# Kernel optimization log

Hardware: AMD Instinct MI355X
Metric: run time of the kernel (lower is better)

## Reference

```python
import jax, jax.numpy as jnp
import numpy as np

N_NODES = 100000
N_EDGES = 1600000
IN_DIM = 128
HID = 128
OUT = 64


def gcn_conv(x, src, dst, W, b, n_nodes):
    # x: [N, Din] -> [N, Dout]; symmetric-normalized GCN with self-loops (PyG GCNConv defaults)
    h = x @ W  # transform first (as PyG does)
    loop = jnp.arange(n_nodes, dtype=src.dtype)
    s = jnp.concatenate([src, loop])
    d = jnp.concatenate([dst, loop])
    deg = jax.ops.segment_sum(jnp.ones_like(d, dtype=h.dtype), d, num_segments=n_nodes)
    dis = jnp.where(deg > 0, jax.lax.rsqrt(deg), 0.0)
    norm = dis[s] * dis[d]  # [E+N]
    msgs = h[s] * norm[:, None]  # gather-transform
    out = jax.ops.segment_sum(msgs, d, num_segments=n_nodes)  # scatter-add
    return out + b


def setup_inputs() -> dict:
    key = jax.random.key(0)
    ks = jax.random.split(key, 12)
    x = jax.random.normal(ks[0], (N_NODES, IN_DIM), dtype=jnp.float32)
    edge_index = jax.random.randint(ks[1], (2, N_EDGES), 0, N_NODES, dtype=jnp.int32)
    def lin(k, fan_in, fan_out):
        bound = 1.0 / np.sqrt(fan_in)
        kw, kb = jax.random.split(k)
        W = jax.random.uniform(kw, (fan_in, fan_out), minval=-bound, maxval=bound, dtype=jnp.float32)
        b = jax.random.uniform(kb, (fan_out,), minval=-bound, maxval=bound, dtype=jnp.float32)
        return W, b
    W1, b1 = lin(ks[2], IN_DIM, HID)
    W2, b2 = lin(ks[3], HID, HID)
    Wp1, bp1 = lin(ks[4], HID, HID)
    Wp2, bp2 = lin(ks[5], HID, OUT)
    return {"x": x, "edge_index": edge_index,
            "W1": W1, "b1": b1, "W2": W2, "b2": b2,
            "Wp1": Wp1, "bp1": bp1, "Wp2": Wp2, "bp2": bp2}


def reference(x, edge_index, W1, b1, W2, b2, Wp1, bp1, Wp2, bp2):
    n = x.shape[0]
    src, dst = edge_index[0], edge_index[1]
    # layer 1: GCNConv + relu (dropout inactive at eval)
    h = jax.nn.relu(gcn_conv(x, src, dst, W1, b1, n))
    # layer 2
    h = jax.nn.relu(gcn_conv(h, src, dst, W2, b2, n))
    # post MLP head
    h = h @ Wp1 + bp1
    h = h @ Wp2 + bp2
    return jax.nn.log_softmax(h, axis=1)
```

## Files before the change

kernel.cpp:

```cpp
#include <hip/hip_runtime.h>
#include <hip/hip_bf16.h>
#include <cstdint>

typedef __attribute__((ext_vector_type(8))) short short8;
typedef __attribute__((ext_vector_type(16))) float f32x16;
typedef unsigned short us;

#define BIN_SHIFT 8
#define BIN_NODES 256
#define CAPB 6144
#define EPB 4096

__device__ __forceinline__ float bflo(uint32_t u) { return __builtin_bit_cast(float, u << 16); }
__device__ __forceinline__ float bfhi(uint32_t u) { return __builtin_bit_cast(float, u & 0xffff0000u); }

__device__ __forceinline__ us f32_to_bf16_rne(float f) {
  uint32_t u = __builtin_bit_cast(uint32_t, f);
  u += 0x7fffu + ((u >> 16) & 1u);
  return (us)(u >> 16);
}

__device__ __forceinline__ void split2(float f, us& h, us& l) {
  uint32_t u = __builtin_bit_cast(uint32_t, f);
  h = (us)(u >> 16);
  float fh = __builtin_bit_cast(float, u & 0xffff0000u);
  float r = f - fh;
  l = (us)(__builtin_bit_cast(uint32_t, r) >> 16);
}

__global__ void k_prep(const float* __restrict__ W1, const float* __restrict__ W2,
                       const float* __restrict__ Wp1, const float* __restrict__ Wp2,
                       const float* __restrict__ bp1, const float* __restrict__ bp2,
                       us* __restrict__ Wt1h, us* __restrict__ Wt1l,
                       us* __restrict__ Wt2h, us* __restrict__ Wt2l,
                       us* __restrict__ Wch, us* __restrict__ Wcl, float* __restrict__ bc,
                       int* __restrict__ gcur, int* __restrict__ hzero) {
  int blk = blockIdx.x, tid = threadIdx.x;
  if (blk < 128) {
    const float* W = (blk < 64) ? W1 : W2;
    us* Wh = (blk < 64) ? Wt1h : Wt2h;
    us* Wl = (blk < 64) ? Wt1l : Wt2l;
    int idx = (blk & 63) * 256 + tid;
    int k = idx >> 7, n = idx & 127;
    us h, l;
    split2(W[idx], h, l);
    Wh[n * 128 + k] = h;
    Wl[n * 128 + k] = l;
  } else if (blk < 160) {
    int idx = (blk - 128) * 256 + tid;
    int k = idx >> 6, j = idx & 63;
    float acc = 0.f;
    for (int t = 0; t < 128; ++t) acc += Wp1[k * 128 + t] * Wp2[t * 64 + j];
    us h, l;
    split2(acc, h, l);
    Wch[j * 128 + k] = h;
    Wcl[j * 128 + k] = l;
  } else {
    gcur[tid] = 0;
    gcur[tid + 256] = 0;
    if (tid < 64) {
      hzero[tid] = 0;
      float acc = bp2[tid];
      for (int t = 0; t < 128; ++t) acc += bp1[t] * Wp2[t * 64 + tid];
      bc[tid] = acc;
    }
  }
}

__global__ __launch_bounds__(256) void k_binA(
    const int* __restrict__ src, const int* __restrict__ dst,
    uint2* __restrict__ binbuf, int* __restrict__ gcur, int E, int nbins) {
  __shared__ uint2 stage[EPB];
  __shared__ int cnt[512], base[512], cur[512], gbase[512];
  int tid = threadIdx.x;
  int e0 = blockIdx.x * EPB;
  int ne = min(EPB, E - e0);
  if (ne <= 0) return;
  cnt[tid] = 0; cnt[tid + 256] = 0;
  __syncthreads();
  for (int i = tid; i < ne; i += 256) atomicAdd(&cnt[dst[e0 + i] >> BIN_SHIFT], 1);
  __syncthreads();
  if (tid < 64) {
    int carry = 0;
#pragma unroll
    for (int c = 0; c < 8; ++c) {
      int v = cnt[c * 64 + tid];
      int incl = v;
#pragma unroll
      for (int off = 1; off < 64; off <<= 1) {
        int t = __shfl_up(incl, off, 64);
        if (tid >= off) incl += t;
      }
      base[c * 64 + tid] = carry + incl - v;
      carry += __shfl(incl, 63, 64);
    }
  }
  __syncthreads();
  for (int b = tid; b < nbins; b += 256)
    if (cnt[b] > 0) gbase[b] = atomicAdd(&gcur[b], cnt[b]);
  cur[tid] = base[tid]; cur[tid + 256] = base[tid + 256];
  __syncthreads();
  for (int i = tid; i < ne; i += 256) {
    int d = dst[e0 + i], s = src[e0 + i];
    int p = atomicAdd(&cur[d >> BIN_SHIFT], 1);
    stage[p] = make_uint2((unsigned)d, (unsigned)s);
  }
  __syncthreads();
  for (int i = tid; i < ne; i += 256) {
    uint2 en = stage[i];
    int b = en.x >> BIN_SHIFT;
    int gi = gbase[b] + (i - base[b]);
    if (gi < CAPB) binbuf[(size_t)b * CAPB + gi] = en;
  }
}

__global__ __launch_bounds__(256) void k_passB(
    const uint2* __restrict__ binbuf, const int* __restrict__ gcur,
    int* __restrict__ deg, float* __restrict__ dis, int* __restrict__ start,
    int* __restrict__ col, int N, int nbins) {
  __shared__ int hist[256], lstart[256], cur[256];
  __shared__ int colstage[CAPB];
  __shared__ int binbase_s;
  int b = blockIdx.x, tid = threadIdx.x;
  int node0 = b << BIN_SHIFT;
  int cnt = min(gcur[b], CAPB);
  hist[tid] = 0;
  __syncthreads();
  const uint2* bp = binbuf + (size_t)b * CAPB;
  for (int i = tid; i < cnt; i += 256) atomicAdd(&hist[bp[i].x & (BIN_NODES - 1)], 1);
  __syncthreads();
  if (tid < 64) {
    int s = 0;
    for (int i = tid; i < b; i += 64) s += min(gcur[i], CAPB);
#pragma unroll
    for (int off = 32; off; off >>= 1) s += __shfl_xor(s, off, 64);
    if (tid == 0) binbase_s = s;
    int carry = 0;
#pragma unroll
    for (int c = 0; c < 4; ++c) {
      int v = hist[c * 64 + tid];
      int incl = v;
#pragma unroll
      for (int off = 1; off < 64; off <<= 1) {
        int t = __shfl_up(incl, off, 64);
        if (tid >= off) incl += t;
      }
      lstart[c * 64 + tid] = carry + incl - v;
      carry += __shfl(incl, 63, 64);
    }
  }
  __syncthreads();
  int binbase = binbase_s;
  {
    int node = node0 + tid;
    if (node < N) {
      int dg = hist[tid];
      deg[node] = dg;
      dis[node] = rsqrtf((float)(dg + 1));
      start[node] = binbase + lstart[tid];
    }
  }
  cur[tid] = lstart[tid];
  __syncthreads();
  for (int i = tid; i < cnt; i += 256) {
    uint2 en = bp[i];
    int p = atomicAdd(&cur[en.x & (BIN_NODES - 1)], 1);
    colstage[p] = (int)en.y;
  }
  __syncthreads();
  for (int i = tid; i < cnt; i += 256) col[binbase + i] = colstage[i];
}

__global__ __launch_bounds__(256) void k_gemm1(
    const float* __restrict__ A, const us* __restrict__ Wh,
    const us* __restrict__ Wl, const float* __restrict__ dis,
    us* __restrict__ out_bf16, int N, int ntiles) {
  __shared__ us As[32 * 136];
  int tid = threadIdx.x;
  int wave = tid >> 6, lane = tid & 63;
  int n0 = wave * 32;
  int nn = n0 + (lane & 31);
  int khalf = (lane >> 5) * 8;
  int m = lane & 31;

  short8 bh[8], bl[8];
#pragma unroll
  for (int c = 0; c < 8; ++c) {
    bh[c] = *(const short8*)&Wh[nn * 128 + c * 16 + khalf];
    bl[c] = *(const short8*)&Wl[nn * 128 + c * 16 + khalf];
  }

  for (int t = blockIdx.x; t < ntiles; t += gridDim.x) {
    int row0 = t * 32;
    __syncthreads();
    for (int j = tid; j < 1024; j += 256) {
      int r = j >> 5, c = j & 31;
      int row = row0 + r;
      float4 v = make_float4(0.f, 0.f, 0.f, 0.f);
      if (row < N) v = *(const float4*)&A[(size_t)row * 128 + c * 4];
      *(ushort4*)&As[r * 136 + c * 4] = make_ushort4(
          f32_to_bf16_rne(v.x), f32_to_bf16_rne(v.y),
          f32_to_bf16_rne(v.z), f32_to_bf16_rne(v.w));
    }
    __syncthreads();

    f32x16 acc = {};
#pragma unroll
    for (int c = 0; c < 8; ++c) {
      short8 ah = *(const short8*)&As[m * 136 + c * 16 + khalf];
      acc = __builtin_amdgcn_mfma_f32_32x32x16_bf16(ah, bh[c], acc, 0, 0, 0);
      acc = __builtin_amdgcn_mfma_f32_32x32x16_bf16(ah, bl[c], acc, 0, 0, 0);
    }

    int col = n0 + (lane & 31);
    int rbase = row0 + 4 * (lane >> 5);
#pragma unroll
    for (int reg = 0; reg < 16; ++reg) {
      int row = rbase + (reg & 3) + 8 * (reg >> 2);
      if (row < N) {
        float v = acc[reg] * dis[row];
        out_bf16[(size_t)row * 128 + col] = f32_to_bf16_rne(v);
      }
    }
  }
}

__global__ __launch_bounds__(256) void k_gemm2(
    const us* __restrict__ A, const us* __restrict__ Wh,
    const us* __restrict__ Wl, const float* __restrict__ dis,
    us* __restrict__ out_bf16, int N, int ntiles) {
  __shared__ us As[32 * 136];
  int tid = threadIdx.x;
  int wave = tid >> 6, lane = tid & 63;
  int n0 = wave * 32;
  int nn = n0 + (lane & 31);
  int khalf = (lane >> 5) * 8;
  int m = lane & 31;

  short8 bh[8], bl[8];
#pragma unroll
  for (int c = 0; c < 8; ++c) {
    bh[c] = *(const short8*)&Wh[nn * 128 + c * 16 + khalf];
    bl[c] = *(const short8*)&Wl[nn * 128 + c * 16 + khalf];
  }

  for (int t = blockIdx.x; t < ntiles; t += gridDim.x) {
    int row0 = t * 32;
    __syncthreads();
    for (int j = tid; j < 512; j += 256) {
      int r = j >> 4, c = j & 15;
      int row = row0 + r;
      uint4 v = make_uint4(0u, 0u, 0u, 0u);
      if (row < N) v = *(const uint4*)&A[(size_t)row * 128 + c * 8];
      *(uint4*)&As[r * 136 + c * 8] = v;
    }
    __syncthreads();

    f32x16 acc = {};
#pragma unroll
    for (int c = 0; c < 8; ++c) {
      short8 ah = *(const short8*)&As[m * 136 + c * 16 + khalf];
      acc = __builtin_amdgcn_mfma_f32_32x32x16_bf16(ah, bh[c], acc, 0, 0, 0);
      acc = __builtin_amdgcn_mfma_f32_32x32x16_bf16(ah, bl[c], acc, 0, 0, 0);
    }

    int col = n0 + (lane & 31);
    int rbase = row0 + 4 * (lane >> 5);
#pragma unroll
    for (int reg = 0; reg < 16; ++reg) {
      int row = rbase + (reg & 3) + 8 * (reg >> 2);
      if (row < N) {
        float v = acc[reg] * dis[row];
        out_bf16[(size_t)row * 128 + col] = f32_to_bf16_rne(v);
      }
    }
  }
}

__global__ __launch_bounds__(512) void k_gather(
    const us* __restrict__ h, us* __restrict__ o,
    const int* __restrict__ start, const int* __restrict__ deg,
    const int* __restrict__ col, const float* __restrict__ dis,
    const float* __restrict__ bias, int N) {
  int wave = threadIdx.x >> 6, lane = threadIdx.x & 63;
  int node = blockIdx.x * 8 + wave;
  if (node >= N) return;
  const uint32_t* h1 = (const uint32_t*)h;
  uint32_t u = h1[(size_t)node * 64 + lane];
  float a0 = bflo(u), b0 = bfhi(u);
  float a1 = 0.f, b1 = 0.f, a2 = 0.f, b2 = 0.f, a3 = 0.f, b3 = 0.f;
  float a4 = 0.f, b4 = 0.f, a5 = 0.f, b5 = 0.f, a6 = 0.f, b6 = 0.f, a7 = 0.f, b7 = 0.f;
  int e0 = start[node];
  int dg = deg[node];
  int myc = (lane < dg) ? col[e0 + lane] : N;
  int dgm = min(dg, 64);
  for (int k = 0; k < dgm; k += 8) {
    int c0 = __builtin_amdgcn_readlane(myc, k);
    int c1 = __builtin_amdgcn_readlane(myc, k + 1);
    int c2 = __builtin_amdgcn_readlane(myc, k + 2);
    int c3 = __builtin_amdgcn_readlane(myc, k + 3);
    int c4 = __builtin_amdgcn_readlane(myc, k + 4);
    int c5 = __builtin_amdgcn_readlane(myc, k + 5);
    int c6 = __builtin_amdgcn_readlane(myc, k + 6);
    int c7 = __builtin_amdgcn_readlane(myc, k + 7);
    uint32_t u0 = h1[(size_t)c0 * 64 + lane];
    uint32_t u1 = h1[(size_t)c1 * 64 + lane];
    uint32_t u2 = h1[(size_t)c2 * 64 + lane];
    uint32_t u3 = h1[(size_t)c3 * 64 + lane];
    uint32_t u4 = h1[(size_t)c4 * 64 + lane];
    uint32_t u5 = h1[(size_t)c5 * 64 + lane];
    uint32_t u6 = h1[(size_t)c6 * 64 + lane];
    uint32_t u7 = h1[(size_t)c7 * 64 + lane];
    a0 += bflo(u0); b0 += bfhi(u0);
    a1 += bflo(u1); b1 += bfhi(u1);
    a2 += bflo(u2); b2 += bfhi(u2);
    a3 += bflo(u3); b3 += bfhi(u3);
    a4 += bflo(u4); b4 += bfhi(u4);
    a5 += bflo(u5); b5 += bfhi(u5);
    a6 += bflo(u6); b6 += bfhi(u6);
    a7 += bflo(u7); b7 += bfhi(u7);
  }
  for (int e = e0 + 64; e < e0 + dg; ++e) {
    uint32_t u0 = h1[(size_t)col[e] * 64 + lane];
    a0 += bflo(u0); b0 += bfhi(u0);
  }
  float sc = dis[node];
  float2 bb = ((const float2*)bias)[lane];
  float ax = ((a0 + a1) + (a2 + a3)) + ((a4 + a5) + (a6 + a7));
  float ay = ((b0 + b1) + (b2 + b3)) + ((b4 + b5) + (b6 + b7));
  float rx = fmaxf(ax * sc + bb.x, 0.f);
  float ry = fmaxf(ay * sc + bb.y, 0.f);
  ((uint32_t*)o)[(size_t)node * 64 + lane] =
      ((uint32_t)f32_to_bf16_rne(ry) << 16) | f32_to_bf16_rne(rx);
}

__global__ __launch_bounds__(256) void k_head_mfma(
    const us* __restrict__ act, const us* __restrict__ Wch,
    const us* __restrict__ Wcl, const float* __restrict__ bc,
    float* __restrict__ out, int N) {
  __shared__ us As[64 * 136];
  __shared__ float red[2][2][64];
  int tid = threadIdx.x;
  int wave = tid >> 6, lane = tid & 63;
  int rt = wave >> 1, ct = wave & 1;
  int colj = ct * 32 + (lane & 31);
  int khalf = (lane >> 5) * 8;
  int m = lane & 31;

  short8 bh[8], bl[8];
#pragma unroll
  for (int c = 0; c < 8; ++c) {
    bh[c] = *(const short8*)&Wch[colj * 128 + c * 16 + khalf];
    bl[c] = *(const short8*)&Wcl[colj * 128 + c * 16 + khalf];
  }

  int row0 = blockIdx.x * 64;
  for (int j = tid; j < 1024; j += 256) {
    int r = j >> 4, c = j & 15;
    int row = row0 + r;
    uint4 v = make_uint4(0u, 0u, 0u, 0u);
    if (row < N) v = *(const uint4*)&act[(size_t)row * 128 + c * 8];
    *(uint4*)&As[r * 136 + c * 8] = v;
  }
  __syncthreads();

  f32x16 acc = {};
  int mrow = rt * 32 + m;
#pragma unroll
  for (int c = 0; c < 8; ++c) {
    short8 ah = *(const short8*)&As[mrow * 136 + c * 16 + khalf];
    acc = __builtin_amdgcn_mfma_f32_32x32x16_bf16(ah, bh[c], acc, 0, 0, 0);
    acc = __builtin_amdgcn_mfma_f32_32x32x16_bf16(ah, bl[c], acc, 0, 0, 0);
  }

  float bcv = bc[colj];
  float lg[16], mx[16];
#pragma unroll
  for (int reg = 0; reg < 16; ++reg) {
    lg[reg] = acc[reg] + bcv;
    float v = lg[reg];
#pragma unroll
    for (int off = 16; off > 0; off >>= 1) v = fmaxf(v, __shfl_xor(v, off, 32));
    mx[reg] = v;
  }
  if ((lane & 31) == 0) {
#pragma unroll
    for (int reg = 0; reg < 16; ++reg) {
      int rl = rt * 32 + (reg & 3) + 8 * (reg >> 2) + 4 * (lane >> 5);
      red[0][ct][rl] = mx[reg];
    }
  }
  __syncthreads();

  float ex[16], sm[16];
#pragma unroll
  for (int reg = 0; reg < 16; ++reg) {
    int rl = rt * 32 + (reg & 3) + 8 * (reg >> 2) + 4 * (lane >> 5);
    float rmax = fmaxf(red[0][0][rl], red[0][1][rl]);
    ex[reg] = lg[reg] - rmax;
    float v = expf(ex[reg]);
#pragma unroll
    for (int off = 16; off > 0; off >>= 1) v += __shfl_xor(v, off, 32);
    sm[reg] = v;
  }
  if ((lane & 31) == 0) {
#pragma unroll
    for (int reg = 0; reg < 16; ++reg) {
      int rl = rt * 32 + (reg & 3) + 8 * (reg >> 2) + 4 * (lane >> 5);
      red[1][ct][rl] = sm[reg];
    }
  }
  __syncthreads();

#pragma unroll
  for (int reg = 0; reg < 16; ++reg) {
    int rl = rt * 32 + (reg & 3) + 8 * (reg >> 2) + 4 * (lane >> 5);
    int row = row0 + rl;
    if (row < N) {
      float total = red[1][0][rl] + red[1][1][rl];
      out[(size_t)row * 64 + colj] = ex[reg] - logf(total);
    }
  }
}

extern "C" void kernel_launch(void* const* d_in, const int* in_sizes, int n_in,
                              void* d_out, int out_size, void* d_ws, size_t ws_size,
                              hipStream_t stream) {
  const float* x   = (const float*)d_in[0];
  const int*   ei  = (const int*)d_in[1];
  const float* W1  = (const float*)d_in[2];
  const float* b1  = (const float*)d_in[3];
  const float* W2  = (const float*)d_in[4];
  const float* b2  = (const float*)d_in[5];
  const float* Wp1 = (const float*)d_in[6];
  const float* bp1 = (const float*)d_in[7];
  const float* Wp2 = (const float*)d_in[8];
  const float* bp2 = (const float*)d_in[9];
  float* out = (float*)d_out;

  int N = in_sizes[0] / 128;
  int E = in_sizes[1] / 2;
  const int* src = ei;
  const int* dst = ei + E;
  int nbins = (N + BIN_NODES - 1) >> BIN_SHIFT;

  float* dis   = (float*)d_ws;
  int*   deg   = (int*)(dis + N);
  int*   start = deg + N;
  int*   col   = start + N;
  int*   gcur  = col + ((E + 3) & ~3);
  us* Wt1h = (us*)(gcur + 512);
  us* Wt1l = Wt1h + 16384;
  us* Wt2h = Wt1l + 16384;
  us* Wt2l = Wt2h + 16384;
  us* Wch  = Wt2l + 16384;
  us* Wcl  = Wch + 8192;
  float* bc = (float*)(Wcl + 8192);
  uint2* binbuf = (uint2*)(bc + 80);
  us* hbuf = (us*)(binbuf + (size_t)nbins * CAPB);
  us* act  = hbuf + (size_t)(N + 1) * 128;

  k_prep<<<161, 256, 0, stream>>>(W1, W2, Wp1, Wp2, bp1, bp2,
                                  Wt1h, Wt1l, Wt2h, Wt2l, Wch, Wcl, bc,
                                  gcur, (int*)(hbuf + (size_t)N * 128));

  int ablocks = (E + EPB - 1) / EPB;
  k_binA<<<ablocks, 256, 0, stream>>>(src, dst, binbuf, gcur, E, nbins);
  k_passB<<<nbins, 256, 0, stream>>>(binbuf, gcur, deg, dis, start, col, N, nbins);

  int ntiles = (N + 31) / 32;
  int gemm_grid = ntiles < 1024 ? ntiles : 1024;
  int agblocks = (N + 7) / 8;
  int hblocks = (N + 63) / 64;

  k_gemm1<<<gemm_grid, 256, 0, stream>>>(x, Wt1h, Wt1l, dis, hbuf, N, ntiles);
  k_gather<<<agblocks, 512, 0, stream>>>(hbuf, act, start, deg, col, dis, b1, N);
  k_gemm2<<<gemm_grid, 256, 0, stream>>>(act, Wt2h, Wt2l, dis, hbuf, N, ntiles);
  k_gather<<<agblocks, 512, 0, stream>>>(hbuf, act, start, deg, col, dis, b2, N);
  k_head_mfma<<<hblocks, 256, 0, stream>>>(act, Wch, Wcl, bc, out, N);
}
```

Before: 389.2 us.

## Compute degrees via global atomics early and overlap CSR build with GEMM1

Degree counting moves out of the per-bin pass into extra k_prep blocks that do global atomicAdd on deg, and extra k_binA blocks then compute dis from it. Because dis no longer depends on the CSR pass, that pass and the first GEMM are merged into one launch (k_pg), with separate block ranges, so they run concurrently. This removes a kernel launch and a serialization point, at the cost of 1.6M global atomics and an added memset.

```diff
diff --git a/kernel.cpp b/kernel.cpp
--- a/kernel.cpp
+++ b/kernel.cpp
@@ -34,7 +34,8 @@
                        us* __restrict__ Wt1h, us* __restrict__ Wt1l,
                        us* __restrict__ Wt2h, us* __restrict__ Wt2l,
                        us* __restrict__ Wch, us* __restrict__ Wcl, float* __restrict__ bc,
-                       int* __restrict__ gcur, int* __restrict__ hzero) {
+                       int* __restrict__ gcur, int* __restrict__ hzero,
+                       const int* __restrict__ dst, int* __restrict__ deg, int E) {
   int blk = blockIdx.x, tid = threadIdx.x;
   if (blk < 128) {
     const float* W = (blk < 64) ? W1 : W2;
@@ -55,7 +56,7 @@
     split2(acc, h, l);
     Wch[j * 128 + k] = h;
     Wcl[j * 128 + k] = l;
-  } else {
+  } else if (blk == 160) {
     gcur[tid] = 0;
     gcur[tid + 256] = 0;
     if (tid < 64) {
@@ -64,12 +65,23 @@
       for (int t = 0; t < 128; ++t) acc += bp1[t] * Wp2[t * 64 + tid];
       bc[tid] = acc;
     }
+  } else {
+    int e0 = (blk - 161) * EPB;
+    int ne = min(EPB, E - e0);
+    for (int i = tid; i < ne; i += 256) atomicAdd(&deg[dst[e0 + i]], 1);
   }
 }
 
 __global__ __launch_bounds__(256) void k_binA(
     const int* __restrict__ src, const int* __restrict__ dst,
-    uint2* __restrict__ binbuf, int* __restrict__ gcur, int E, int nbins) {
+    uint2* __restrict__ binbuf, int* __restrict__ gcur,
+    const int* __restrict__ deg, float* __restrict__ dis,
+    int E, int nbins, int ablocks, int N) {
+  if ((int)blockIdx.x >= ablocks) {
+    int i = ((int)blockIdx.x - ablocks) * 256 + (int)threadIdx.x;
+    if (i < N) dis[i] = rsqrtf((float)(deg[i] + 1));
+    return;
+  }
   __shared__ uint2 stage[EPB];
   __shared__ int cnt[512], base[512], cur[512], gbase[512];
   int tid = threadIdx.x;
@@ -114,112 +126,106 @@
   }
 }
 
-__global__ __launch_bounds__(256) void k_passB(
+__global__ __launch_bounds__(256) void k_pg(
     const uint2* __restrict__ binbuf, const int* __restrict__ gcur,
-    int* __restrict__ deg, float* __restrict__ dis, int* __restrict__ start,
-    int* __restrict__ col, int N, int nbins) {
-  __shared__ int hist[256], lstart[256], cur[256];
-  __shared__ int colstage[CAPB];
-  __shared__ int binbase_s;
-  int b = blockIdx.x, tid = threadIdx.x;
-  int node0 = b << BIN_SHIFT;
-  int cnt = min(gcur[b], CAPB);
-  hist[tid] = 0;
-  __syncthreads();
-  const uint2* bp = binbuf + (size_t)b * CAPB;
-  for (int i = tid; i < cnt; i += 256) atomicAdd(&hist[bp[i].x & (BIN_NODES - 1)], 1);
-  __syncthreads();
-  if (tid < 64) {
-    int s = 0;
-    for (int i = tid; i < b; i += 64) s += min(gcur[i], CAPB);
-#pragma unroll
-    for (int off = 32; off; off >>= 1) s += __shfl_xor(s, off, 64);
-    if (tid == 0) binbase_s = s;
-    int carry = 0;
-#pragma unroll
-    for (int c = 0; c < 4; ++c) {
-      int v = hist[c * 64 + tid];
-      int incl = v;
-#pragma unroll
-      for (int off = 1; off < 64; off <<= 1) {
-        int t = __shfl_up(incl, off, 64);
-        if (tid >= off) incl += t;
-      }
-      lstart[c * 64 + tid] = carry + incl - v;
-      carry += __shfl(incl, 63, 64);
-    }
-  }
-  __syncthreads();
-  int binbase = binbase_s;
-  {
+    const int* __restrict__ deg, int* __restrict__ start, int* __restrict__ col,
+    const float* __restrict__ A, const us* __restrict__ Wh, const us* __restrict__ Wl,
+    const float* __restrict__ dis, us* __restrict__ out_bf16,
+    int N, int nbins, int ntiles) {
+  __shared__ int lds[6913];
+  int tid = threadIdx.x;
+  if ((int)blockIdx.x < nbins) {
+    int b = blockIdx.x;
+    int* hist = lds;
+    int* lstart = lds + 256;
+    int* cur = lds + 512;
+    int* colstage = lds + 768;
+    int node0 = b << BIN_SHIFT;
+    int cnt = min(gcur[b], CAPB);
     int node = node0 + tid;
-    if (node < N) {
-      int dg = hist[tid];
-      deg[node] = dg;
-      dis[node] = rsqrtf((float)(dg + 1));
-      start[node] = binbase + lstart[tid];
-    }
-  }
-  cur[tid] = lstart[tid];
-  __syncthreads();
-  for (int i = tid; i < cnt; i += 256) {
-    uint2 en = bp[i];
-    int p = atomicAdd(&cur[en.x & (BIN_NODES - 1)], 1);
-    colstage[p] = (int)en.y;
-  }
-  __syncthreads();
-  for (int i = tid; i < cnt; i += 256) col[binbase + i] = colstage[i];
-}
-
-__global__ __launch_bounds__(256) void k_gemm1(
-    const float* __restrict__ A, const us* __restrict__ Wh,
-    const us* __restrict__ Wl, const float* __restrict__ dis,
-    us* __restrict__ out_bf16, int N, int ntiles) {
-  __shared__ us As[32 * 136];
-  int tid = threadIdx.x;
-  int wave = tid >> 6, lane = tid & 63;
-  int n0 = wave * 32;
-  int nn = n0 + (lane & 31);
-  int khalf = (lane >> 5) * 8;
-  int m = lane & 31;
-
-  short8 bh[8], bl[8];
-#pragma unroll
-  for (int c = 0; c < 8; ++c) {
-    bh[c] = *(const short8*)&Wh[nn * 128 + c * 16 + khalf];
-    bl[c] = *(const short8*)&Wl[nn * 128 + c * 16 + khalf];
-  }
-
-  for (int t = blockIdx.x; t < ntiles; t += gridDim.x) {
-    int row0 = t * 32;
-    __syncthreads();
-    for (int j = tid; j < 1024; j += 256) {
-      int r = j >> 5, c = j & 31;
-      int row = row0 + r;
-      float4 v = make_float4(0.f, 0.f, 0.f, 0.f);
-      if (row < N) v = *(const float4*)&A[(size_t)row * 128 + c * 4];
-      *(ushort4*)&As[r * 136 + c * 4] = make_ushort4(
-          f32_to_bf16_rne(v.x), f32_to_bf16_rne(v.y),
-          f32_to_bf16_rne(v.z), f32_to_bf16_rne(v.w));
-    }
-    __syncthreads();
-
-    f32x16 acc = {};
+    hist[tid] = (node < N) ? deg[node] : 0;
+    __syncthreads();
+    if (tid < 64) {
+      int s = 0;
+      for (int i = tid; i < b; i += 64) s += min(gcur[i], CAPB);
+#pragma unroll
+      for (int off = 32; off; off >>= 1) s += __shfl_xor(s, off, 64);
+      if (tid == 0) lds[6912] = s;
+      int carry = 0;
+#pragma unroll
+      for (int c = 0; c < 4; ++c) {
+        int v = hist[c * 64 + tid];
+        int incl = v;
+#pragma unroll
+        for (int off = 1; off < 64; off <<= 1) {
+          int t = __shfl_up(incl, off, 64);
+          if (tid >= off) incl += t;
+        }
+        lstart[c * 64 + tid] = carry + incl - v;
+        carry += __shfl(incl, 63, 64);
+      }
+    }
+    __syncthreads();
+    int binbase = lds[6912];
+    if (node < N) start[node] = binbase + lstart[tid];
+    cur[tid] = lstart[tid];
+    __syncthreads();
+    const uint2* bp = binbuf + (size_t)b * CAPB;
+    for (int i = tid; i < cnt; i += 256) {
+      uint2 en = bp[i];
+      int p = atomicAdd(&cur[en.x & (BIN_NODES - 1)], 1);
+      colstage[p] = (int)en.y;
+    }
+    __syncthreads();
+    for (int i = tid; i < cnt; i += 256) col[binbase + i] = colstage[i];
+  } else {
+    us* As = (us*)lds;
+    int wave = tid >> 6, lane = tid & 63;
+    int n0 = wave * 32;
+    int nn = n0 + (lane & 31);
+    int khalf = (lane >> 5) * 8;
+    int m = lane & 31;
+
+    short8 bh[8], bl[8];
 #pragma unroll
     for (int c = 0; c < 8; ++c) {
-      short8 ah = *(const short8*)&As[m * 136 + c * 16 + khalf];
-      acc = __builtin_amdgcn_mfma_f32_32x32x16_bf16(ah, bh[c], acc, 0, 0, 0);
-      acc = __builtin_amdgcn_mfma_f32_32x32x16_bf16(ah, bl[c], acc, 0, 0, 0);
-    }
-
-    int col = n0 + (lane & 31);
-    int rbase = row0 + 4 * (lane >> 5);
-#pragma unroll
-    for (int reg = 0; reg < 16; ++reg) {
-      int row = rbase + (reg & 3) + 8 * (reg >> 2);
-      if (row < N) {
-        float v = acc[reg] * dis[row];
-        out_bf16[(size_t)row * 128 + col] = f32_to_bf16_rne(v);
+      bh[c] = *(const short8*)&Wh[nn * 128 + c * 16 + khalf];
+      bl[c] = *(const short8*)&Wl[nn * 128 + c * 16 + khalf];
+    }
+
+    int t0 = (int)blockIdx.x - nbins;
+    int nstride = (int)gridDim.x - nbins;
+    for (int t = t0; t < ntiles; t += nstride) {
+      int row0 = t * 32;
+      __syncthreads();
+      for (int j = tid; j < 1024; j += 256) {
+        int r = j >> 5, c = j & 31;
+        int row = row0 + r;
+        float4 v = make_float4(0.f, 0.f, 0.f, 0.f);
+        if (row < N) v = *(const float4*)&A[(size_t)row * 128 + c * 4];
+        *(ushort4*)&As[r * 136 + c * 4] = make_ushort4(
+            f32_to_bf16_rne(v.x), f32_to_bf16_rne(v.y),
+            f32_to_bf16_rne(v.z), f32_to_bf16_rne(v.w));
+      }
+      __syncthreads();
+
+      f32x16 acc = {};
+#pragma unroll
+      for (int c = 0; c < 8; ++c) {
+        short8 ah = *(const short8*)&As[m * 136 + c * 16 + khalf];
+        acc = __builtin_amdgcn_mfma_f32_32x32x16_bf16(ah, bh[c], acc, 0, 0, 0);
+        acc = __builtin_amdgcn_mfma_f32_32x32x16_bf16(ah, bl[c], acc, 0, 0, 0);
+      }
+
+      int colo = n0 + (lane & 31);
+      int rbase = row0 + 4 * (lane >> 5);
+#pragma unroll
+      for (int reg = 0; reg < 16; ++reg) {
+        int row = rbase + (reg & 3) + 8 * (reg >> 2);
+        if (row < N) {
+          float v = acc[reg] * dis[row];
+          out_bf16[(size_t)row * 128 + colo] = f32_to_bf16_rne(v);
+        }
       }
     }
   }
@@ -460,20 +466,24 @@
   us* hbuf = (us*)(binbuf + (size_t)nbins * CAPB);
   us* act  = hbuf + (size_t)(N + 1) * 128;
 
-  k_prep<<<161, 256, 0, stream>>>(W1, W2, Wp1, Wp2, bp1, bp2,
-                                  Wt1h, Wt1l, Wt2h, Wt2l, Wch, Wcl, bc,
-                                  gcur, (int*)(hbuf + (size_t)N * 128));
+  hipMemsetAsync(deg, 0, N * sizeof(int), stream);
 
   int ablocks = (E + EPB - 1) / EPB;
-  k_binA<<<ablocks, 256, 0, stream>>>(src, dst, binbuf, gcur, E, nbins);
-  k_passB<<<nbins, 256, 0, stream>>>(binbuf, gcur, deg, dis, start, col, N, nbins);
-
+  int dblocks = (N + 255) / 256;
   int ntiles = (N + 31) / 32;
   int gemm_grid = ntiles < 1024 ? ntiles : 1024;
   int agblocks = (N + 7) / 8;
   int hblocks = (N + 63) / 64;
 
-  k_gemm1<<<gemm_grid, 256, 0, stream>>>(x, Wt1h, Wt1l, dis, hbuf, N, ntiles);
+  k_prep<<<161 + ablocks, 256, 0, stream>>>(W1, W2, Wp1, Wp2, bp1, bp2,
+                                            Wt1h, Wt1l, Wt2h, Wt2l, Wch, Wcl, bc,
+                                            gcur, (int*)(hbuf + (size_t)N * 128),
+                                            dst, deg, E);
+  k_binA<<<ablocks + dblocks, 256, 0, stream>>>(src, dst, binbuf, gcur, deg, dis,
+                                                E, nbins, ablocks, N);
+  k_pg<<<nbins + gemm_grid, 256, 0, stream>>>(binbuf, gcur, deg, start, col,
+                                              x, Wt1h, Wt1l, dis, hbuf,
+                                              N, nbins, ntiles);
   k_gather<<<agblocks, 512, 0, stream>>>(hbuf, act, start, deg, col, dis, b1, N);
   k_gemm2<<<gemm_grid, 256, 0, stream>>>(act, Wt2h, Wt2l, dis, hbuf, N, ntiles);
   k_gather<<<agblocks, 512, 0, stream>>>(hbuf, act, start, deg, col, dis, b2, N);
```

After: 449.2 us. 1.15x slower.

## Fuse edge binning with first GEMM and move dis scaling into gather

Applied to the files above, without the earlier changes.

Edge binning and the layer-1 GEMM now run as one launch: the first blocks bin edges and the remaining 1024 blocks run the GEMM. Because the GEMM no longer depends on degrees, the source-side dis scaling moves into a new first-layer gather kernel that multiplies each neighbor's value by dis[col]. Bin entries are packed into 32 bits (local node in the top 8 bits, source in the low 24), which halves binning traffic but assumes node ids below 2^24. The new gather adds a dis lookup per edge, and the fused kernel uses a larger shared-memory footprint that may lower occupancy.

```diff
diff --git a/kernel.cpp b/kernel.cpp
--- a/kernel.cpp
+++ b/kernel.cpp
@@ -10,6 +10,7 @@
 #define BIN_NODES 256
 #define CAPB 6144
 #define EPB 4096
+#define G1GRID 1024
 
 __device__ __forceinline__ float bflo(uint32_t u) { return __builtin_bit_cast(float, u << 16); }
 __device__ __forceinline__ float bfhi(uint32_t u) { return __builtin_bit_cast(float, u & 0xffff0000u); }
@@ -18,6 +19,10 @@
   uint32_t u = __builtin_bit_cast(uint32_t, f);
   u += 0x7fffu + ((u >> 16) & 1u);
   return (us)(u >> 16);
+}
+
+__device__ __forceinline__ float rdlane_f(float v, int l) {
+  return __builtin_bit_cast(float, __builtin_amdgcn_readlane(__builtin_bit_cast(int, v), l));
 }
 
 __device__ __forceinline__ void split2(float f, us& h, us& l) {
@@ -67,55 +72,111 @@
   }
 }
 
-__global__ __launch_bounds__(256) void k_binA(
+__global__ __launch_bounds__(256) void k_bg(
     const int* __restrict__ src, const int* __restrict__ dst,
-    uint2* __restrict__ binbuf, int* __restrict__ gcur, int E, int nbins) {
-  __shared__ uint2 stage[EPB];
-  __shared__ int cnt[512], base[512], cur[512], gbase[512];
+    uint32_t* __restrict__ binbuf, int* __restrict__ gcur, int E, int nbins, int ablocks,
+    const float* __restrict__ A, const us* __restrict__ Wh, const us* __restrict__ Wl,
+    us* __restrict__ out_bf16, int N, int ntiles) {
+  __shared__ int smem[10240];
   int tid = threadIdx.x;
-  int e0 = blockIdx.x * EPB;
-  int ne = min(EPB, E - e0);
-  if (ne <= 0) return;
-  cnt[tid] = 0; cnt[tid + 256] = 0;
-  __syncthreads();
-  for (int i = tid; i < ne; i += 256) atomicAdd(&cnt[dst[e0 + i] >> BIN_SHIFT], 1);
-  __syncthreads();
-  if (tid < 64) {
-    int carry = 0;
+  if ((int)blockIdx.x < ablocks) {
+    uint2* stage = (uint2*)smem;
+    int* cnt   = smem + 8192;
+    int* base  = smem + 8704;
+    int* cur   = smem + 9216;
+    int* gbase = smem + 9728;
+    int e0 = blockIdx.x * EPB;
+    int ne = min(EPB, E - e0);
+    if (ne <= 0) return;
+    cnt[tid] = 0; cnt[tid + 256] = 0;
+    __syncthreads();
+    for (int i = tid; i < ne; i += 256) atomicAdd(&cnt[dst[e0 + i] >> BIN_SHIFT], 1);
+    __syncthreads();
+    if (tid < 64) {
+      int carry = 0;
+#pragma unroll
+      for (int c = 0; c < 8; ++c) {
+        int v = cnt[c * 64 + tid];
+        int incl = v;
+#pragma unroll
+        for (int off = 1; off < 64; off <<= 1) {
+          int t = __shfl_up(incl, off, 64);
+          if (tid >= off) incl += t;
+        }
+        base[c * 64 + tid] = carry + incl - v;
+        carry += __shfl(incl, 63, 64);
+      }
+    }
+    __syncthreads();
+    for (int b = tid; b < nbins; b += 256)
+      if (cnt[b] > 0) gbase[b] = atomicAdd(&gcur[b], cnt[b]);
+    cur[tid] = base[tid]; cur[tid + 256] = base[tid + 256];
+    __syncthreads();
+    for (int i = tid; i < ne; i += 256) {
+      int d = dst[e0 + i], s = src[e0 + i];
+      int p = atomicAdd(&cur[d >> BIN_SHIFT], 1);
+      stage[p] = make_uint2((unsigned)d, (unsigned)s);
+    }
+    __syncthreads();
+    for (int i = tid; i < ne; i += 256) {
+      uint2 en = stage[i];
+      int b = en.x >> BIN_SHIFT;
+      int gi = gbase[b] + (i - base[b]);
+      if (gi < CAPB)
+        binbuf[(size_t)b * CAPB + gi] = ((en.x & (BIN_NODES - 1)) << 24) | en.y;
+    }
+  } else {
+    us* As = (us*)smem;
+    int wave = tid >> 6, lane = tid & 63;
+    int n0 = wave * 32;
+    int nn = n0 + (lane & 31);
+    int khalf = (lane >> 5) * 8;
+    int m = lane & 31;
+
+    short8 bh[8], bl[8];
 #pragma unroll
     for (int c = 0; c < 8; ++c) {
-      int v = cnt[c * 64 + tid];
-      int incl = v;
-#pragma unroll
-      for (int off = 1; off < 64; off <<= 1) {
-        int t = __shfl_up(incl, off, 64);
-        if (tid >= off) incl += t;
+      bh[c] = *(const short8*)&Wh[nn * 128 + c * 16 + khalf];
+      bl[c] = *(const short8*)&Wl[nn * 128 + c * 16 + khalf];
+    }
+
+    int t0 = (int)blockIdx.x - ablocks;
+    for (int t = t0; t < ntiles; t += G1GRID) {
+      int row0 = t * 32;
+      __syncthreads();
+      for (int j = tid; j < 1024; j += 256) {
+        int r = j >> 5, c = j & 31;
+        int row = row0 + r;
+        float4 v = make_float4(0.f, 0.f, 0.f, 0.f);
+        if (row < N) v = *(const float4*)&A[(size_t)row * 128 + c * 4];
+        *(ushort4*)&As[r * 136 + c * 4] = make_ushort4(
+            f32_to_bf16_rne(v.x), f32_to_bf16_rne(v.y),
+            f32_to_bf16_rne(v.z), f32_to_bf16_rne(v.w));
       }
-      base[c * 64 + tid] = carry + incl - v;
-      carry += __shfl(incl, 63, 64);
-    }
-  }
-  __syncthreads();
-  for (int b = tid; b < nbins; b += 256)
-    if (cnt[b] > 0) gbase[b] = atomicAdd(&gcur[b], cnt[b]);
-  cur[tid] = base[tid]; cur[tid + 256] = base[tid + 256];
-  __syncthreads();
-  for (int i = tid; i < ne; i += 256) {
-    int d = dst[e0 + i], s = src[e0 + i];
-    int p = atomicAdd(&cur[d >> BIN_SHIFT], 1);
-    stage[p] = make_uint2((unsigned)d, (unsigned)s);
-  }
-  __syncthreads();
-  for (int i = tid; i < ne; i += 256) {
-    uint2 en = stage[i];
-    int b = en.x >> BIN_SHIFT;
-    int gi = gbase[b] + (i - base[b]);
-    if (gi < CAPB) binbuf[(size_t)b * CAPB + gi] = en;
+      __syncthreads();
+
+      f32x16 acc = {};
+#pragma unroll
+      for (int c = 0; c < 8; ++c) {
+        short8 ah = *(const short8*)&As[m * 136 + c * 16 + khalf];
+        acc = __builtin_amdgcn_mfma_f32_32x32x16_bf16(ah, bh[c], acc, 0, 0, 0);
+        acc = __builtin_amdgcn_mfma_f32_32x32x16_bf16(ah, bl[c], acc, 0, 0, 0);
+      }
+
+      int colo = n0 + (lane & 31);
+      int rbase = row0 + 4 * (lane >> 5);
+#pragma unroll
+      for (int reg = 0; reg < 16; ++reg) {
+        int row = rbase + (reg & 3) + 8 * (reg >> 2);
+        if (row < N)
+          out_bf16[(size_t)row * 128 + colo] = f32_to_bf16_rne(acc[reg]);
+      }
+    }
   }
 }
 
 __global__ __launch_bounds__(256) void k_passB(
-    const uint2* __restrict__ binbuf, const int* __restrict__ gcur,
+    const uint32_t* __restrict__ binbuf, const int* __restrict__ gcur,
     int* __restrict__ deg, float* __restrict__ dis, int* __restrict__ start,
     int* __restrict__ col, int N, int nbins) {
   __shared__ int hist[256], lstart[256], cur[256];
@@ -126,8 +187,8 @@
   int cnt = min(gcur[b], CAPB);
   hist[tid] = 0;
   __syncthreads();
-  const uint2* bp = binbuf + (size_t)b * CAPB;
-  for (int i = tid; i < cnt; i += 256) atomicAdd(&hist[bp[i].x & (BIN_NODES - 1)], 1);
+  const uint32_t* bp = binbuf + (size_t)b * CAPB;
+  for (int i = tid; i < cnt; i += 256) atomicAdd(&hist[bp[i] >> 24], 1);
   __syncthreads();
   if (tid < 64) {
     int s = 0;
@@ -163,66 +224,76 @@
   cur[tid] = lstart[tid];
   __syncthreads();
   for (int i = tid; i < cnt; i += 256) {
-    uint2 en = bp[i];
-    int p = atomicAdd(&cur[en.x & (BIN_NODES - 1)], 1);
-    colstage[p] = (int)en.y;
+    uint32_t en = bp[i];
+    int p = atomicAdd(&cur[en >> 24], 1);
+    colstage[p] = (int)(en & 0xFFFFFFu);
   }
   __syncthreads();
   for (int i = tid; i < cnt; i += 256) col[binbase + i] = colstage[i];
 }
 
-__global__ __launch_bounds__(256) void k_gemm1(
-    const float* __restrict__ A, const us* __restrict__ Wh,
-    const us* __restrict__ Wl, const float* __restrict__ dis,
-    us* __restrict__ out_bf16, int N, int ntiles) {
-  __shared__ us As[32 * 136];
-  int tid = threadIdx.x;
-  int wave = tid >> 6, lane = tid & 63;
-  int n0 = wave * 32;
-  int nn = n0 + (lane & 31);
-  int khalf = (lane >> 5) * 8;
-  int m = lane & 31;
-
-  short8 bh[8], bl[8];
-#pragma unroll
-  for (int c = 0; c < 8; ++c) {
-    bh[c] = *(const short8*)&Wh[nn * 128 + c * 16 + khalf];
-    bl[c] = *(const short8*)&Wl[nn * 128 + c * 16 + khalf];
-  }
-
-  for (int t = blockIdx.x; t < ntiles; t += gridDim.x) {
-    int row0 = t * 32;
-    __syncthreads();
-    for (int j = tid; j < 1024; j += 256) {
-      int r = j >> 5, c = j & 31;
-      int row = row0 + r;
-      float4 v = make_float4(0.f, 0.f, 0.f, 0.f);
-      if (row < N) v = *(const float4*)&A[(size_t)row * 128 + c * 4];
-      *(ushort4*)&As[r * 136 + c * 4] = make_ushort4(
-          f32_to_bf16_rne(v.x), f32_to_bf16_rne(v.y),
-          f32_to_bf16_rne(v.z), f32_to_bf16_rne(v.w));
-    }
-    __syncthreads();
-
-    f32x16 acc = {};
-#pragma unroll
-    for (int c = 0; c < 8; ++c) {
-      short8 ah = *(const short8*)&As[m * 136 + c * 16 + khalf];
-      acc = __builtin_amdgcn_mfma_f32_32x32x16_bf16(ah, bh[c], acc, 0, 0, 0);
-      acc = __builtin_amdgcn_mfma_f32_32x32x16_bf16(ah, bl[c], acc, 0, 0, 0);
-    }
-
-    int col = n0 + (lane & 31);
-    int rbase = row0 + 4 * (lane >> 5);
-#pragma unroll
-    for (int reg = 0; reg < 16; ++reg) {
-      int row = rbase + (reg & 3) + 8 * (reg >> 2);
-      if (row < N) {
-        float v = acc[reg] * dis[row];
-        out_bf16[(size_t)row * 128 + col] = f32_to_bf16_rne(v);
-      }
-    }
-  }
+__global__ __launch_bounds__(512) void k_gather1(
+    const us* __restrict__ h, us* __restrict__ o,
+    const int* __restrict__ start, const int* __restrict__ deg,
+    const int* __restrict__ col, const float* __restrict__ dis,
+    const float* __restrict__ bias, int N) {
+  int wave = threadIdx.x >> 6, lane = threadIdx.x & 63;
+  int node = blockIdx.x * 8 + wave;
+  if (node >= N) return;
+  const uint32_t* h1 = (const uint32_t*)h;
+  float sc = dis[node];
+  uint32_t u = h1[(size_t)node * 64 + lane];
+  float a0 = sc * bflo(u), b0 = sc * bfhi(u);
+  float a1 = 0.f, b1 = 0.f, a2 = 0.f, b2 = 0.f, a3 = 0.f, b3 = 0.f;
+  float a4 = 0.f, b4 = 0.f, a5 = 0.f, b5 = 0.f, a6 = 0.f, b6 = 0.f, a7 = 0.f, b7 = 0.f;
+  int e0 = start[node];
+  int dg = deg[node];
+  int myc = (lane < dg) ? col[e0 + lane] : N;
+  float myd = (lane < dg) ? dis[myc] : 0.f;
+  int dgm = min(dg, 64);
+  for (int k = 0; k < dgm; k += 8) {
+    int c0 = __builtin_amdgcn_readlane(myc, k);
+    int c1 = __builtin_amdgcn_readlane(myc, k + 1);
+    int c2 = __builtin_amdgcn_readlane(myc, k + 2);
+    int c3 = __builtin_amdgcn_readlane(myc, k + 3);
+    int c4 = __builtin_amdgcn_readlane(myc, k + 4);
+    int c5 = __builtin_amdgcn_readlane(myc, k + 5);
+    int c6 = __builtin_amdgcn_readlane(myc, k + 6);
+    int c7 = __builtin_amdgcn_readlane(myc, k + 7);
+    float d0 = rdlane_f(myd, k),     d1 = rdlane_f(myd, k + 1);
+    float d2 = rdlane_f(myd, k + 2), d3 = rdlane_f(myd, k + 3);
+    float d4 = rdlane_f(myd, k + 4), d5 = rdlane_f(myd, k + 5);
+    float d6 = rdlane_f(myd, k + 6), d7 = rdlane_f(myd, k + 7);
+    uint32_t u0 = h1[(size_t)c0 * 64 + lane];
+    uint32_t u1 = h1[(size_t)c1 * 64 + lane];
+    uint32_t u2 = h1[(size_t)c2 * 64 + lane];
+    uint32_t u3 = h1[(size_t)c3 * 64 + lane];
+    uint32_t u4 = h1[(size_t)c4 * 64 + lane];
+    uint32_t u5 = h1[(size_t)c5 * 64 + lane];
+    uint32_t u6 = h1[(size_t)c6 * 64 + lane];
+    uint32_t u7 = h1[(size_t)c7 * 64 + lane];
+    a0 += d0 * bflo(u0); b0 += d0 * bfhi(u0);
+    a1 += d1 * bflo(u1); b1 += d1 * bfhi(u1);
+    a2 += d2 * bflo(u2); b2 += d2 * bfhi(u2);
+    a3 += d3 * bflo(u3); b3 += d3 * bfhi(u3);
+    a4 += d4 * bflo(u4); b4 += d4 * bfhi(u4);
+    a5 += d5 * bflo(u5); b5 += d5 * bfhi(u5);
+    a6 += d6 * bflo(u6); b6 += d6 * bfhi(u6);
+    a7 += d7 * bflo(u7); b7 += d7 * bfhi(u7);
+  }
+  for (int e = e0 + 64; e < e0 + dg; ++e) {
+    int c = col[e];
+    float dd = dis[c];
+    uint32_t u0 = h1[(size_t)c * 64 + lane];
+    a0 += dd * bflo(u0); b0 += dd * bfhi(u0);
+  }
+  float2 bb = ((const float2*)bias)[lane];
+  float ax = ((a0 + a1) + (a2 + a3)) + ((a4 + a5) + (a6 + a7));
+  float ay = ((b0 + b1) + (b2 + b3)) + ((b4 + b5) + (b6 + b7));
+  float rx = fmaxf(ax * sc + bb.x, 0.f);
+  float ry = fmaxf(ay * sc + bb.y, 0.f);
+  ((uint32_t*)o)[(size_t)node * 64 + lane] =
+      ((uint32_t)f32_to_bf16_rne(ry) << 16) | f32_to_bf16_rne(rx);
 }
 
 __global__ __launch_bounds__(256) void k_gemm2(
@@ -456,26 +527,24 @@
   us* Wch  = Wt2l + 16384;
   us* Wcl  = Wch + 8192;
   float* bc = (float*)(Wcl + 8192);
-  uint2* binbuf = (uint2*)(bc + 80);
+  uint32_t* binbuf = (uint32_t*)(bc + 80);
   us* hbuf = (us*)(binbuf + (size_t)nbins * CAPB);
   us* act  = hbuf + (size_t)(N + 1) * 128;
+
+  int ablocks = (E + EPB - 1) / EPB;
+  int ntiles = (N + 31) / 32;
+  int agblocks = (N + 7) / 8;
+  int hblocks = (N + 63) / 64;
 
   k_prep<<<161, 256, 0, stream>>>(W1, W2, Wp1, Wp2, bp1, bp2,
                                   Wt1h, Wt1l, Wt2h, Wt2l, Wch, Wcl, bc,
                                   gcur, (int*)(hbuf + (size_t)N * 128));
-
-  int ablocks = (E + EPB - 1) / EPB;
-  k_binA<<<ablocks, 256, 0, stream>>>(src, dst, binbuf, gcur, E, nbins);
+  k_bg<<<ablocks + G1GRID, 256, 0, stream>>>(src, dst, binbuf, gcur, E, nbins, ablocks,
+                                             x, Wt1h, Wt1l, hbuf, N, ntiles);
   k_passB<<<nbins, 256, 0, stream>>>(binbuf, gcur, deg, dis, start, col, N, nbins);
 
-  int ntiles = (N + 31) / 32;
-  int gemm_grid = ntiles < 1024 ? ntiles : 1024;
-  int agblocks = (N + 7) / 8;
-  int hblocks = (N + 63) / 64;
-
-  k_gemm1<<<gemm_grid, 256, 0, stream>>>(x, Wt1h, Wt1l, dis, hbuf, N, ntiles);
-  k_gather<<<agblocks, 512, 0, stream>>>(hbuf, act, start, deg, col, dis, b1, N);
-  k_gemm2<<<gemm_grid, 256, 0, stream>>>(act, Wt2h, Wt2l, dis, hbuf, N, ntiles);
+  k_gather1<<<agblocks, 512, 0, stream>>>(hbuf, act, start, deg, col, dis, b1, N);
+  k_gemm2<<<ntiles < 1024 ? ntiles : 1024, 256, 0, stream>>>(act, Wt2h, Wt2l, dis, hbuf, N, ntiles);
   k_gather<<<agblocks, 512, 0, stream>>>(hbuf, act, start, deg, col, dis, b2, N);
   k_head_mfma<<<hblocks, 256, 0, stream>>>(act, Wch, Wcl, bc, out, N);
 }
```

Measured after the change: 373.4 us. 4.1% less time.
